# Performance work log

Measured on AMD Instinct MI355X. Metric: run time of the kernel, lower is better.

The kernel has to match this reference:

```python
import jax, jax.numpy as jnp
import numpy as np

T = 1_000_000  # sequence length
H = 5          # LSTM hidden size
NC = 4         # number of channel streams (all fed through lstm1, as in the original)


def setup_inputs() -> dict:
    key = jax.random.key(0)
    ks = jax.random.split(key, 14)
    s = 1.0 / np.sqrt(H)  # PyTorch default LSTM/Linear init scale
    u = lambda k, shape: jax.random.uniform(k, shape, jnp.float32, -s, s)
    sf1 = 1.0 / np.sqrt(20.0)
    sf2 = 1.0 / np.sqrt(10.0)
    return {
        "inputs": jax.random.normal(ks[0], (T, 1, NC), jnp.float32),
        # lstm1 layer 0: input_size=1
        "w_ih0": u(ks[1], (4 * H, 1)),
        "w_hh0": u(ks[2], (4 * H, H)),
        "b_ih0": u(ks[3], (4 * H,)),
        "b_hh0": u(ks[4], (4 * H,)),
        # lstm1 layer 1: input_size=H
        "w_ih1": u(ks[5], (4 * H, H)),
        "w_hh1": u(ks[6], (4 * H, H)),
        "b_ih1": u(ks[7], (4 * H,)),
        "b_hh1": u(ks[8], (4 * H,)),
        "fc1_w": jax.random.uniform(ks[9], (10, 20), jnp.float32, -sf1, sf1),
        "fc1_b": jax.random.uniform(ks[10], (10,), jnp.float32, -sf1, sf1),
        "fc2_w": jax.random.uniform(ks[11], (1, 10), jnp.float32, -sf2, sf2),
        "fc2_b": jax.random.uniform(ks[12], (1,), jnp.float32, -sf2, sf2),
    }


def _lstm_layer(x_seq, w_ih, w_hh, b_ih, b_hh):
    """Single PyTorch-style LSTM layer. x_seq: (T, B, in) -> h_seq: (T, B, H)."""
    # Input projection for all timesteps at once (outside the scan).
    gx = jnp.einsum('tbi,gi->tbg', x_seq, w_ih) + b_ih + b_hh  # (T, B, 4H)

    def step(carry, gx_t):
        h, c = carry
        g = gx_t + h @ w_hh.T                      # (B, 4H)
        i, f, gg, o = jnp.split(g, 4, axis=-1)     # PyTorch gate order i,f,g,o
        i = jax.nn.sigmoid(i)
        f = jax.nn.sigmoid(f)
        gg = jnp.tanh(gg)
        o = jax.nn.sigmoid(o)
        c = f * c + i * gg
        h = o * jnp.tanh(c)
        return (h, c), h

    B = x_seq.shape[1]
    z = jnp.zeros((B, H), x_seq.dtype)
    _, h_seq = jax.lax.scan(step, (z, z), gx)
    return h_seq


def reference(inputs, w_ih0, w_hh0, b_ih0, b_hh0, w_ih1, w_hh1, b_ih1, b_hh1,
              fc1_w, fc1_b, fc2_w, fc2_b):
    # Original code runs all 4 channel streams through lstm1 (lstm2-4 unused),
    # so we fold the 4 streams into the LSTM batch dim: (T, 4, 1).
    x = inputs[:, 0, :, None]                      # (T, NC, 1)
    h = _lstm_layer(x, w_ih0, w_hh0, b_ih0, b_hh0)  # (T, NC, H)
    h = _lstm_layer(h, w_ih1, w_hh1, b_ih1, b_hh1)  # (T, NC, H)
    # torch.cat((out1..out4), dim=2) on (T,1,H) slices == channel-major reshape
    out_cat = h.reshape(T, 1, NC * H)              # (T, 1, 20)
    out = out_cat @ fc1_w.T + fc1_b                # (T, 1, 10)
    out = out @ fc2_w.T + fc2_b                    # (T, 1, 1)
    return out
```

## Files before the change

kernel.cpp:

```cpp
#include <hip/hip_runtime.h>

#define T_TOTAL 1000000
#define NCHUNK  9216
#define CLEN    109
#define WARM    24


typedef float v2 __attribute__((ext_vector_type(2)));

#define L2E  1.44269504088896340736f
#define K2   2.88539008177792681472f

__device__ __forceinline__ float bperm(int addr4, float v) {
    return __int_as_float(__builtin_amdgcn_ds_bpermute(addr4, __float_as_int(v)));
}
__device__ __forceinline__ v2 pkfma(v2 a, v2 b, v2 c) {
    return __builtin_elementwise_fma(a, b, c);
}

__device__ __forceinline__ void cell(v2 A01, v2 A23, float& C, float& h) {
    const float ei = __builtin_amdgcn_exp2f(A01.x);
    const float ef = __builtin_amdgcn_exp2f(A01.y);
    const float eg = __builtin_amdgcn_exp2f(A23.x);
    const float eo = __builtin_amdgcn_exp2f(A23.y);
    const float Di = 1.0f + ei, Df = 1.0f + ef, Dg = 1.0f + eg, Do = 1.0f + eo;
    const float p1 = Di * Df, p2 = Dg * Do, p3 = Df * Do;
    const float r  = __builtin_amdgcn_rcpf(p1 * p2);
    const float f  = (Di * p2) * r;
    const float o  = (p1 * Dg) * r;
    const float tg = __builtin_fmaf(K2, eg, -K2);
    C = __builtin_fmaf(f, C, (tg * p3) * r);
    const float eh = __builtin_amdgcn_exp2f(C);
    h = (o * (1.0f - eh)) * __builtin_amdgcn_rcpf(1.0f + eh);
}

__global__ __launch_bounds__(64, 1) void lstm_chunks(
    const float* __restrict__ inp,
    const float* __restrict__ wih0,
    const float* __restrict__ whh0,
    const float* __restrict__ bih0,
    const float* __restrict__ bhh0,
    const float* __restrict__ wih1,
    const float* __restrict__ whh1,
    const float* __restrict__ bih1,
    const float* __restrict__ bhh1,
    const float* __restrict__ fc1w,
    const float* __restrict__ fc1b,
    const float* __restrict__ fc2w,
    const float* __restrict__ fc2b,
    float* __restrict__ out)
{
    const int lane = threadIdx.x & 63;
    int cw = lane / 20; if (cw > 2) cw = 2;
    int q  = lane - cw * 20; if (q > 19) q = 19;
    const int b = q / 5;
    const int j = q % 5;
    const int chunk = blockIdx.x * 3 + cw;
    const int base  = cw * 20;

    int gh[5];
    #pragma unroll
    for (int k = 0; k < 5; ++k) gh[k] = (base + b * 5 + k) * 4;
    const int rd5  = (lane + 5)  * 4;
    const int rd10 = (lane + 10) * 4;

    v2 W0x01, W0x23, BB001, BB023, BB101, BB123;
    v2 W0h01[5], W0h23[5], W1a01[5], W1a23[5], W1b01[5], W1b23[5];
    {
        const int r0 = j, r1 = 5 + j, r2 = 10 + j, r3 = 15 + j;
        const v2 s01 = v2{-L2E, -L2E};
        const v2 s23 = v2{-K2,  -L2E};
        W0x01 = s01 * v2{wih0[r0], wih0[r1]};
        W0x23 = s23 * v2{wih0[r2], wih0[r3]};
        BB001 = s01 * v2{bih0[r0] + bhh0[r0], bih0[r1] + bhh0[r1]};
        BB023 = s23 * v2{bih0[r2] + bhh0[r2], bih0[r3] + bhh0[r3]};
        BB101 = s01 * v2{bih1[r0] + bhh1[r0], bih1[r1] + bhh1[r1]};
        BB123 = s23 * v2{bih1[r2] + bhh1[r2], bih1[r3] + bhh1[r3]};
        #pragma unroll
        for (int k = 0; k < 5; ++k) {
            W0h01[k] = s01 * v2{whh0[r0 * 5 + k], whh0[r1 * 5 + k]};
            W0h23[k] = s23 * v2{whh0[r2 * 5 + k], whh0[r3 * 5 + k]};
            W1a01[k] = s01 * v2{wih1[r0 * 5 + k], wih1[r1 * 5 + k]};
            W1a23[k] = s23 * v2{wih1[r2 * 5 + k], wih1[r3 * 5 + k]};
            W1b01[k] = s01 * v2{whh1[r0 * 5 + k], whh1[r1 * 5 + k]};
            W1b23[k] = s23 * v2{whh1[r2 * 5 + k], whh1[r3 * 5 + k]};
        }
    }
    float vb[5] = {0, 0, 0, 0, 0};
    float sc = fc2b[0];
    #pragma unroll
    for (int m = 0; m < 10; ++m) {
        const float f2 = fc2w[m];
        sc = __builtin_fmaf(f2, fc1b[m], sc);
        #pragma unroll
        for (int k = 0; k < 5; ++k)
            vb[k] = __builtin_fmaf(f2, fc1w[m * 20 + b * 5 + k], vb[k]);
    }

    const int o_begin = chunk * CLEN;
    const int warm = (chunk == 0) ? 0 : WARM;

    float C0 = 0.0f, C1 = 0.0f, h0 = 0.0f, h1 = 0.0f;
    float h0r[5] = {0, 0, 0, 0, 0};
    float h1r[5] = {0, 0, 0, 0, 0};

    auto ldx = [&](int t) -> float {
        const int tt = (t > T_TOTAL - 1) ? (T_TOTAL - 1) : t;
        return inp[(size_t)tt * 4 + b];
    };

    auto recur = [&](float x) {
        v2 A01, A23, P01, P23, Q01, Q23;
        {
            const v2 xx = v2{x, x};
            P01 = pkfma(W0x01, xx, BB001);
            P23 = pkfma(W0x23, xx, BB023);
            const v2 k0 = v2{h0r[0], h0r[0]}, k1 = v2{h0r[1], h0r[1]};
            const v2 k2 = v2{h0r[2], h0r[2]}, k3 = v2{h0r[3], h0r[3]};
            const v2 k4 = v2{h0r[4], h0r[4]};
            P01 = pkfma(W0h01[0], k0, P01);  Q01 = W0h01[2] * k2;
            P23 = pkfma(W0h23[0], k0, P23);  Q23 = W0h23[2] * k2;
            P01 = pkfma(W0h01[1], k1, P01);  Q01 = pkfma(W0h01[3], k3, Q01);
            P23 = pkfma(W0h23[1], k1, P23);  Q23 = pkfma(W0h23[3], k3, Q23);
            Q01 = pkfma(W0h01[4], k4, Q01);
            Q23 = pkfma(W0h23[4], k4, Q23);
            A01 = P01 + Q01; A23 = P23 + Q23;
        }
        cell(A01, A23, C0, h0);
        #pragma unroll
        for (int k = 0; k < 5; ++k) h0r[k] = bperm(gh[k], h0);
        {
            P01 = BB101; P23 = BB123;
            const v2 g0 = v2{h1r[0], h1r[0]};
            Q01 = W1b01[0] * g0;
            Q23 = W1b23[0] * g0;
            #pragma unroll
            for (int k = 0; k < 5; ++k) {
                const v2 hk = v2{h0r[k], h0r[k]};
                P01 = pkfma(W1a01[k], hk, P01);
                P23 = pkfma(W1a23[k], hk, P23);
            }
            #pragma unroll
            for (int k = 1; k < 5; ++k) {
                const v2 gk = v2{h1r[k], h1r[k]};
                Q01 = pkfma(W1b01[k], gk, Q01);
                Q23 = pkfma(W1b23[k], gk, Q23);
            }
            A01 = P01 + Q01; A23 = P23 + Q23;
        }
        cell(A01, A23, C1, h1);
        #pragma unroll
        for (int k = 0; k < 5; ++k) h1r[k] = bperm(gh[k], h1);
    };

    int t = o_begin - warm;
    float xc = ldx(t);
    for (int i = 0; i < warm; ++i, ++t) {
        const float xn = ldx(t + 1);
        recur(xc);
        xc = xn;
    }
    for (int i = 0; i < CLEN; ++i, ++t) {
        const float xn = ldx(t + 1);
        recur(xc);
        xc = xn;
        float p = vb[0] * h1r[0];
        p = __builtin_fmaf(vb[1], h1r[1], p);
        p = __builtin_fmaf(vb[2], h1r[2], p);
        p = __builtin_fmaf(vb[3], h1r[3], p);
        p = __builtin_fmaf(vb[4], h1r[4], p);
        const float u = p + bperm(rd5, p);
        const float S = u + bperm(rd10, u);
        if (q == 0 && t < T_TOTAL) out[t] = S + sc;
    }
}

extern "C" void kernel_launch(void* const* d_in, const int* in_sizes, int n_in,
                              void* d_out, int out_size, void* d_ws, size_t ws_size,
                              hipStream_t stream) {
    (void)in_sizes; (void)n_in; (void)d_ws; (void)ws_size; (void)out_size;
    lstm_chunks<<<NCHUNK / 3, 64, 0, stream>>>(
        (const float*)d_in[0],  (const float*)d_in[1],  (const float*)d_in[2],
        (const float*)d_in[3],  (const float*)d_in[4],  (const float*)d_in[5],
        (const float*)d_in[6],  (const float*)d_in[7],  (const float*)d_in[8],
        (const float*)d_in[9],  (const float*)d_in[10], (const float*)d_in[11],
        (const float*)d_in[12], (float*)d_out);
}
```

Baseline: 194.1 us.

## Software-pipeline LSTM layers so layer1 step t overlaps layer0 step t+1

Restructures the per-step recurrence so that each loop iteration computes layer 1 for time t and layer 0 for time t+1, which are independent. Layer 0 gets a one-step prologue. This gives the scheduler two independent dependency chains to interleave, hiding transcendental and bpermute latency in a latency-bound single-wave kernel. The cost is slightly more live registers and a shifted input prefetch.

```diff
diff --git a/kernel.cpp b/kernel.cpp
--- a/kernel.cpp
+++ b/kernel.cpp
@@ -16,22 +16,6 @@
 }
 __device__ __forceinline__ v2 pkfma(v2 a, v2 b, v2 c) {
     return __builtin_elementwise_fma(a, b, c);
-}
-
-__device__ __forceinline__ void cell(v2 A01, v2 A23, float& C, float& h) {
-    const float ei = __builtin_amdgcn_exp2f(A01.x);
-    const float ef = __builtin_amdgcn_exp2f(A01.y);
-    const float eg = __builtin_amdgcn_exp2f(A23.x);
-    const float eo = __builtin_amdgcn_exp2f(A23.y);
-    const float Di = 1.0f + ei, Df = 1.0f + ef, Dg = 1.0f + eg, Do = 1.0f + eo;
-    const float p1 = Di * Df, p2 = Dg * Do, p3 = Df * Do;
-    const float r  = __builtin_amdgcn_rcpf(p1 * p2);
-    const float f  = (Di * p2) * r;
-    const float o  = (p1 * Dg) * r;
-    const float tg = __builtin_fmaf(K2, eg, -K2);
-    C = __builtin_fmaf(f, C, (tg * p3) * r);
-    const float eh = __builtin_amdgcn_exp2f(C);
-    h = (o * (1.0f - eh)) * __builtin_amdgcn_rcpf(1.0f + eh);
 }
 
 __global__ __launch_bounds__(64, 1) void lstm_chunks(
@@ -100,7 +84,7 @@
     const int o_begin = chunk * CLEN;
     const int warm = (chunk == 0) ? 0 : WARM;
 
-    float C0 = 0.0f, C1 = 0.0f, h0 = 0.0f, h1 = 0.0f;
+    float C0 = 0.0f, C1 = 0.0f;
     float h0r[5] = {0, 0, 0, 0, 0};
     float h1r[5] = {0, 0, 0, 0, 0};
 
@@ -109,70 +93,99 @@
         return inp[(size_t)tt * 4 + b];
     };
 
-    auto recur = [&](float x) {
-        v2 A01, A23, P01, P23, Q01, Q23;
-        {
-            const v2 xx = v2{x, x};
-            P01 = pkfma(W0x01, xx, BB001);
-            P23 = pkfma(W0x23, xx, BB023);
-            const v2 k0 = v2{h0r[0], h0r[0]}, k1 = v2{h0r[1], h0r[1]};
-            const v2 k2 = v2{h0r[2], h0r[2]}, k3 = v2{h0r[3], h0r[3]};
-            const v2 k4 = v2{h0r[4], h0r[4]};
-            P01 = pkfma(W0h01[0], k0, P01);  Q01 = W0h01[2] * k2;
-            P23 = pkfma(W0h23[0], k0, P23);  Q23 = W0h23[2] * k2;
-            P01 = pkfma(W0h01[1], k1, P01);  Q01 = pkfma(W0h01[3], k3, Q01);
-            P23 = pkfma(W0h23[1], k1, P23);  Q23 = pkfma(W0h23[3], k3, Q23);
-            Q01 = pkfma(W0h01[4], k4, Q01);
-            Q23 = pkfma(W0h23[4], k4, Q23);
-            A01 = P01 + Q01; A23 = P23 + Q23;
+    auto cellp = [&](v2 A01, v2 A23, float& C) -> float {
+        const float ei = __builtin_amdgcn_exp2f(A01.x);
+        const float ef = __builtin_amdgcn_exp2f(A01.y);
+        const float eg = __builtin_amdgcn_exp2f(A23.x);
+        const float eo = __builtin_amdgcn_exp2f(A23.y);
+        const float Di = 1.0f + ei, Df = 1.0f + ef, Dg = 1.0f + eg, Do = 1.0f + eo;
+        const float p1 = Di * Df, p2 = Dg * Do, p3 = Df * Do;
+        const float r  = __builtin_amdgcn_rcpf(p1 * p2);
+        const float f  = (Di * p2) * r;
+        const float o  = (p1 * Dg) * r;
+        const float tg = __builtin_fmaf(K2, eg, -K2);
+        C = __builtin_fmaf(f, C, (tg * p3) * r);
+        const float eh = __builtin_amdgcn_exp2f(C);
+        return (o * (1.0f - eh)) * __builtin_amdgcn_rcpf(1.0f + eh);
+    };
+
+    auto matvec0 = [&](float x, const float (&h)[5], v2& A01, v2& A23) {
+        const v2 xx = v2{x, x};
+        v2 P01 = pkfma(W0x01, xx, BB001);
+        v2 P23 = pkfma(W0x23, xx, BB023);
+        const v2 k0 = v2{h[0], h[0]}, k1 = v2{h[1], h[1]};
+        const v2 k2 = v2{h[2], h[2]}, k3 = v2{h[3], h[3]};
+        const v2 k4 = v2{h[4], h[4]};
+        P01 = pkfma(W0h01[0], k0, P01);  v2 Q01 = W0h01[2] * k2;
+        P23 = pkfma(W0h23[0], k0, P23);  v2 Q23 = W0h23[2] * k2;
+        P01 = pkfma(W0h01[1], k1, P01);  Q01 = pkfma(W0h01[3], k3, Q01);
+        P23 = pkfma(W0h23[1], k1, P23);  Q23 = pkfma(W0h23[3], k3, Q23);
+        Q01 = pkfma(W0h01[4], k4, Q01);
+        Q23 = pkfma(W0h23[4], k4, Q23);
+        A01 = P01 + Q01; A23 = P23 + Q23;
+    };
+    auto matvec1 = [&](const float (&h0)[5], const float (&h1)[5], v2& A01, v2& A23) {
+        v2 P01 = BB101, P23 = BB123;
+        const v2 g0 = v2{h1[0], h1[0]};
+        v2 Q01 = W1b01[0] * g0;
+        v2 Q23 = W1b23[0] * g0;
+        #pragma unroll
+        for (int k = 0; k < 5; ++k) {
+            const v2 hk = v2{h0[k], h0[k]};
+            P01 = pkfma(W1a01[k], hk, P01);
+            P23 = pkfma(W1a23[k], hk, P23);
         }
-        cell(A01, A23, C0, h0);
+        #pragma unroll
+        for (int k = 1; k < 5; ++k) {
+            const v2 gk = v2{h1[k], h1[k]};
+            Q01 = pkfma(W1b01[k], gk, Q01);
+            Q23 = pkfma(W1b23[k], gk, Q23);
+        }
+        A01 = P01 + Q01; A23 = P23 + Q23;
+    };
+
+    int t = o_begin - warm;
+    {
+        v2 A01, A23;
+        matvec0(ldx(t), h0r, A01, A23);
+        const float h0 = cellp(A01, A23, C0);
         #pragma unroll
         for (int k = 0; k < 5; ++k) h0r[k] = bperm(gh[k], h0);
-        {
-            P01 = BB101; P23 = BB123;
-            const v2 g0 = v2{h1r[0], h1r[0]};
-            Q01 = W1b01[0] * g0;
-            Q23 = W1b23[0] * g0;
-            #pragma unroll
-            for (int k = 0; k < 5; ++k) {
-                const v2 hk = v2{h0r[k], h0r[k]};
-                P01 = pkfma(W1a01[k], hk, P01);
-                P23 = pkfma(W1a23[k], hk, P23);
-            }
-            #pragma unroll
-            for (int k = 1; k < 5; ++k) {
-                const v2 gk = v2{h1r[k], h1r[k]};
-                Q01 = pkfma(W1b01[k], gk, Q01);
-                Q23 = pkfma(W1b23[k], gk, Q23);
-            }
-            A01 = P01 + Q01; A23 = P23 + Q23;
-        }
-        cell(A01, A23, C1, h1);
-        #pragma unroll
-        for (int k = 0; k < 5; ++k) h1r[k] = bperm(gh[k], h1);
-    };
-
-    int t = o_begin - warm;
-    float xc = ldx(t);
-    for (int i = 0; i < warm; ++i, ++t) {
-        const float xn = ldx(t + 1);
-        recur(xc);
-        xc = xn;
-    }
-    for (int i = 0; i < CLEN; ++i, ++t) {
-        const float xn = ldx(t + 1);
-        recur(xc);
-        xc = xn;
-        float p = vb[0] * h1r[0];
-        p = __builtin_fmaf(vb[1], h1r[1], p);
-        p = __builtin_fmaf(vb[2], h1r[2], p);
-        p = __builtin_fmaf(vb[3], h1r[3], p);
-        p = __builtin_fmaf(vb[4], h1r[4], p);
-        const float u = p + bperm(rd5, p);
-        const float S = u + bperm(rd10, u);
-        if (q == 0 && t < T_TOTAL) out[t] = S + sc;
-    }
+    }
+    float xc = ldx(t + 1);
+
+    #define BODY(EMIT)                                                         \
+    {                                                                          \
+        v2 A01, A23;                                                           \
+        matvec1(h0r, h1r, A01, A23);                                           \
+        const float h1 = cellp(A01, A23, C1);                                  \
+        float h1n[5];                                                          \
+        _Pragma("unroll")                                                      \
+        for (int k = 0; k < 5; ++k) h1n[k] = bperm(gh[k], h1);                 \
+        const float xn = ldx(t + 2);                                           \
+        matvec0(xc, h0r, A01, A23);                                            \
+        const float h0 = cellp(A01, A23, C0);                                  \
+        _Pragma("unroll")                                                      \
+        for (int k = 0; k < 5; ++k) h0r[k] = bperm(gh[k], h0);                 \
+        xc = xn;                                                               \
+        if (EMIT) {                                                            \
+            float p = vb[0] * h1n[0];                                          \
+            p = __builtin_fmaf(vb[1], h1n[1], p);                              \
+            p = __builtin_fmaf(vb[2], h1n[2], p);                              \
+            p = __builtin_fmaf(vb[3], h1n[3], p);                              \
+            p = __builtin_fmaf(vb[4], h1n[4], p);                              \
+            const float u = p + bperm(rd5, p);                                 \
+            const float S = u + bperm(rd10, u);                                \
+            if (q == 0 && t < T_TOTAL) out[t] = S + sc;                        \
+        }                                                                      \
+        _Pragma("unroll")                                                      \
+        for (int k = 0; k < 5; ++k) h1r[k] = h1n[k];                           \
+    }
+
+    for (int i = 0; i < warm; ++i, ++t) BODY(false)
+    for (int i = 0; i < CLEN; ++i, ++t) BODY(true)
+
+    #undef BODY
 }
 
 extern "C" void kernel_launch(void* const* d_in, const int* in_sizes, int n_in,
```

Measured after the change: 181.0 us. -6.7%, faster.
